# Kernel optimization log

Hardware: AMD Instinct MI355X
Metric: run time of the kernel (lower is better)

Reference implementation:

```python
import jax, jax.numpy as jnp
import numpy as np

N = 100000
E = 1600000
BN_EPS = 1e-5
# (in_channels, heads, out_channels, concat) per GATv2 layer
LAYERS = [(22, 3, 18, True), (54, 3, 14, True), (42, 3, 12, True), (36, 5, 10, False)]


def setup_inputs() -> dict:
    key = jax.random.key(0)
    ks = iter(jax.random.split(key, 64))
    nrm = lambda shape, s=0.1: jax.random.normal(next(ks), shape, jnp.float32) * s
    d = {}
    d["x"] = jax.random.normal(next(ks), (N, 22), jnp.float32)
    d["edge_index"] = jax.random.randint(next(ks), (2, E), 0, N)
    for i, (cin, h, c, concat) in enumerate(LAYERS, 1):
        d[f"Wl{i}"] = nrm((cin, h * c))
        d[f"Wr{i}"] = nrm((cin, h * c))
        d[f"bl{i}"] = jnp.zeros((h * c,), jnp.float32)
        d[f"br{i}"] = jnp.zeros((h * c,), jnp.float32)
        d[f"att{i}"] = nrm((h, c))
        outd = h * c if concat else c
        d[f"b{i}"] = jnp.zeros((outd,), jnp.float32)
        d[f"g{i}"] = jnp.ones((outd,), jnp.float32)
        d[f"be{i}"] = jnp.zeros((outd,), jnp.float32)
        d[f"rm{i}"] = nrm((outd,))
        d[f"rv{i}"] = jax.random.uniform(next(ks), (outd,), jnp.float32, 0.5, 1.5)
    d["Wmu"] = nrm((10, 10)); d["bmu"] = jnp.zeros((10,), jnp.float32)
    d["Wlv"] = nrm((10, 10)); d["blv"] = jnp.zeros((10,), jnp.float32)
    return d


def _gatv2(x, Wl, Wr, bl, br, att, b, src, dst, H, C, concat):
    n = x.shape[0]
    xl = (x @ Wl + bl).reshape(n, H, C)  # source transform (also the message)
    xr = (x @ Wr + br).reshape(n, H, C)  # target transform
    m = jax.nn.leaky_relu(xl[src] + xr[dst], 0.2)          # [Etot, H, C]
    e = jnp.einsum('ehc,hc->eh', m, att)                   # [Etot, H]
    emax = jax.lax.stop_gradient(jax.ops.segment_max(e, dst, num_segments=n))
    ex = jnp.exp(e - emax[dst])
    den = jax.ops.segment_sum(ex, dst, num_segments=n)     # [n, H]
    alpha = ex / den[dst]
    out = jax.ops.segment_sum(xl[src] * alpha[..., None], dst, num_segments=n)
    out = out.reshape(n, H * C) if concat else out.mean(axis=1)
    return out + b


def _bn(x, g, be, rm, rv):
    return g * (x - rm) * jax.lax.rsqrt(rv + BN_EPS) + be


def _fwd(p, edge_index):
    n = p["x"].shape[0]
    loop = jnp.arange(n)  # PyG GATv2Conv adds self-loops by default
    src = jnp.concatenate([edge_index[0], loop])
    dst = jnp.concatenate([edge_index[1], loop])
    h = p["x"]
    for i, (cin, H, C, concat) in enumerate(LAYERS, 1):
        h = _gatv2(h, p[f"Wl{i}"], p[f"Wr{i}"], p[f"bl{i}"], p[f"br{i}"],
                   p[f"att{i}"], p[f"b{i}"], src, dst, H, C, concat)
        h = _bn(h, p[f"g{i}"], p[f"be{i}"], p[f"rm{i}"], p[f"rv{i}"])
        if i == 1:  # source applies ELU only after bn1
            h = jax.nn.elu(h)
    mu = h @ p["Wmu"] + p["bmu"]
    log_var = h @ p["Wlv"] + p["blv"]
    return mu, log_var


def reference(x, edge_index, Wl1, Wr1, bl1, br1, att1, b1, g1, be1, rm1, rv1, Wl2, Wr2, bl2, br2, att2, b2, g2, be2, rm2, rv2, Wl3, Wr3, bl3, br3, att3, b3, g3, be3, rm3, rv3, Wl4, Wr4, bl4, br4, att4, b4, g4, be4, rm4, rv4, Wmu, bmu, Wlv, blv):
    p = {k: v for k, v in locals().items() if k != "edge_index"}
    return _fwd(p, edge_index)
```

## Files before the change

kernel.cpp:

```cpp
#include <hip/hip_runtime.h>

#define BN_EPS 1e-5f

typedef _Float16 half_t;
typedef _Float16 half2_t __attribute__((ext_vector_type(2)));

#define NBK_MAX 512
#define EPB 4096
#define REC 64
#define CAP 5120


__global__ void __launch_bounds__(256) bucket_scatter_kernel(
    const int* __restrict__ ei, int* __restrict__ bcur, int2* __restrict__ bstage,
    int E, int etot, int nbk) {
  __shared__ int2 se[EPB];
  __shared__ int lh[NBK_MAX], lbase[NBK_MAX];
  int base = blockIdx.x * EPB;
  int cnt = min(EPB, etot - base);
  for (int i = threadIdx.x; i < nbk; i += 256) lh[i] = 0;
  __syncthreads();
  for (int i = threadIdx.x; i < cnt; i += 256) {
    int e = base + i;
    int s, d;
    if (e < E) { s = ei[e]; d = ei[E + e]; } else { s = e - E; d = s; }
    se[i] = make_int2(s, d);
    atomicAdd(&lh[d >> 8], 1);
  }
  __syncthreads();
  for (int i = threadIdx.x; i < nbk; i += 256) {
    int c = lh[i];
    lbase[i] = c ? (i * CAP + atomicAdd(&bcur[i], c)) : 0;
    lh[i] = 0;
  }
  __syncthreads();
  for (int i = threadIdx.x; i < cnt; i += 256) {
    int2 sd = se[i];
    int b = sd.y >> 8;
    int r = atomicAdd(&lh[b], 1);
    bstage[lbase[b] + r] = sd;
  }
}

__global__ void __launch_bounds__(256) csr_finalize_kernel(
    const int2* __restrict__ bstage, const int* __restrict__ bcur,
    int* __restrict__ start, int* __restrict__ deg, int* __restrict__ csrc, int n) {
  __shared__ int ld[256];
  __shared__ int wsum[4];
  int b = blockIdx.x, tid = threadIdx.x;
  int d0 = b << 8;
  int p0 = b * CAP;
  int bc = bcur[b];
  ld[tid] = 0;
  __syncthreads();
  for (int p = p0 + tid; p < p0 + bc; p += 256)
    atomicAdd(&ld[bstage[p].y - d0], 1);
  __syncthreads();
  int v = ld[tid];
  int lane = tid & 63, wid = tid >> 6;
  int incl = v;
#pragma unroll
  for (int off = 1; off < 64; off <<= 1) {
    int t = __shfl_up(incl, off, 64);
    if (lane >= off) incl += t;
  }
  if (lane == 63) wsum[wid] = incl;
  __syncthreads();
  if (tid == 0) {
    int s = 0;
#pragma unroll
    for (int w = 0; w < 4; w++) { int t = wsum[w]; wsum[w] = s; s += t; }
  }
  __syncthreads();
  incl += wsum[wid];
  int st = p0 + incl - v;
  int i = d0 + tid;
  if (i < n) { start[i] = st; deg[i] = v; }
  __syncthreads();
  ld[tid] = st;
  __syncthreads();
  for (int p = p0 + tid; p < p0 + bc; p += 256) {
    int2 sd = bstage[p];
    int pos = atomicAdd(&ld[sd.y - d0], 1);
    csrc[pos] = sd.x;
  }
}


template <int CIN, int H, int C, int JT, typename IT>
__global__ void __launch_bounds__(256) transform_kernel(
    const IT* __restrict__ x, const float* __restrict__ Wl, const float* __restrict__ Wr,
    const float* __restrict__ bl, const float* __restrict__ br, half_t* __restrict__ xl,
    half_t* __restrict__ xr, int n) {
  constexpr int HC = H * C;
  constexpr int TPN = HC / JT;
  __shared__ float sW[2 * CIN * HC];
  for (int i = threadIdx.x; i < CIN * HC; i += blockDim.x) {
    sW[i] = Wl[i];
    sW[CIN * HC + i] = Wr[i];
  }
  __syncthreads();
  int idx = blockIdx.x * blockDim.x + threadIdx.x;
  if (idx >= n * TPN) return;
  int node = idx / TPN;
  int j0 = (idx - node * TPN) * JT;

  float al[JT], ar[JT];
#pragma unroll
  for (int jj = 0; jj < JT; jj++) {
    al[jj] = bl[j0 + jj];
    ar[jj] = br[j0 + jj];
  }
  float xrow[CIN];
  if constexpr (sizeof(IT) == 4) {
    const float2* xp = reinterpret_cast<const float2*>((const float*)x + (size_t)node * CIN);
#pragma unroll
    for (int k2 = 0; k2 < CIN / 2; k2++) {
      float2 v = xp[k2];
      xrow[2 * k2] = v.x;
      xrow[2 * k2 + 1] = v.y;
    }
  } else {
    const half2_t* xp = reinterpret_cast<const half2_t*>((const half_t*)x + (size_t)node * CIN);
#pragma unroll
    for (int k2 = 0; k2 < CIN / 2; k2++) {
      half2_t v = xp[k2];
      xrow[2 * k2] = (float)v.x;
      xrow[2 * k2 + 1] = (float)v.y;
    }
  }
#pragma unroll
  for (int k = 0; k < CIN; k++) {
    float xs = xrow[k];
#pragma unroll
    for (int jj = 0; jj < JT; jj++) {
      al[jj] = fmaf(xs, sW[k * HC + j0 + jj], al[jj]);
      ar[jj] = fmaf(xs, sW[CIN * HC + k * HC + j0 + jj], ar[jj]);
    }
  }
#pragma unroll
  for (int jj = 0; jj < JT; jj++) {
    int j = j0 + jj;
    xl[(size_t)node * REC + j] = (half_t)al[jj];
    xr[(size_t)node * HC + j] = (half_t)ar[jj];
  }
}


#define IDX(K) csrc[p0 + (((K) < cnt) ? (K) : cnt - 1)]

#define ROW(B, IR)                                                                  \
  {                                                                                 \
    const uint* xp_ = reinterpret_cast<const uint*>(xlh + (size_t)(IR) * REC);      \
    _Pragma("unroll") for (int i_ = 0; i_ < C2; i_++) B[i_] = xp_[i_];              \
  }

#define COMP_ROW(B, M)                                                                      \
  {                                                                                         \
    const half2_t* hp_ = reinterpret_cast<const half2_t*>(B);                               \
    float xs_[C];                                                                           \
    _Pragma("unroll") for (int i = 0; i < C2; i++) {                                        \
      xs_[2 * i] = (float)hp_[i].x;                                                         \
      xs_[2 * i + 1] = (float)hp_[i].y;                                                     \
    }                                                                                       \
    float e_ = 0.f;                                                                         \
    _Pragma("unroll") for (int c = 0; c < C; c++) {                                         \
      float m_ = xs_[c] + xr_reg[c];                                                        \
      m_ = (m_ > 0.f) ? m_ : 0.2f * m_;                                                     \
      e_ = fmaf(att_reg[c], m_, e_);                                                        \
    }                                                                                       \
    float ex_ = ((M) < cnt) ? __expf(e_) : 0.f;                                             \
    den += ex_;                                                                             \
    _Pragma("unroll") for (int c = 0; c < C; c++) acc[c] = fmaf(ex_, xs_[c], acc[c]);       \
  }

template <int H, int C, int MODE>
__global__ void __launch_bounds__(256) edge_kernel(
    const half_t* __restrict__ xl, const half_t* __restrict__ xr,
    const int* __restrict__ start, const int* __restrict__ deg,
    const int* __restrict__ csrc, const float* __restrict__ att,
    const float* __restrict__ bias, const float* __restrict__ g,
    const float* __restrict__ be, const float* __restrict__ rm,
    const float* __restrict__ rv, half_t* __restrict__ out, int n) {
  constexpr int HC = H * C;
  constexpr int C2 = C / 2;
  int t = blockIdx.x * blockDim.x + threadIdx.x;
  if (t >= n * H) return;
  int node = t / H;
  int h = t - node * H;

  float xr_reg[C], att_reg[C];
  const half2_t* xrp = reinterpret_cast<const half2_t*>(xr + (size_t)node * HC + h * C);
#pragma unroll
  for (int i = 0; i < C2; i++) {
    half2_t v = xrp[i];
    xr_reg[2 * i] = (float)v.x;
    xr_reg[2 * i + 1] = (float)v.y;
  }
#pragma unroll
  for (int c = 0; c < C; c++) att_reg[c] = att[h * C + c];

  float acc[C];
#pragma unroll
  for (int c = 0; c < C; c++) acc[c] = 0.f;
  float den = 0.f;

  int p0 = start[node];
  int cnt = deg[node];
  const half_t* xlh = xl + h * C;

  uint B0[C2], B1[C2], B2[C2];
  int i0, i1, i2;
  i0 = IDX(0); i1 = IDX(1); i2 = IDX(2);
  ROW(B0, i0) ROW(B1, i1) ROW(B2, i2)
  i0 = IDX(3); i1 = IDX(4); i2 = IDX(5);
  int cnt3 = ((cnt + 2) / 3) * 3;
  for (int m = 0; m < cnt3; m += 3) {
    COMP_ROW(B0, m)     ROW(B0, i0) i0 = IDX(m + 6);
    COMP_ROW(B1, m + 1) ROW(B1, i1) i1 = IDX(m + 7);
    COMP_ROW(B2, m + 2) ROW(B2, i2) i2 = IDX(m + 8);
  }

  float inv = 1.f / den;
  uint* orow = reinterpret_cast<uint*>(out + (size_t)node * HC + h * C);
#pragma unroll
  for (int c2 = 0; c2 < C2; c2++) {
    half2_t ov;
#pragma unroll
    for (int q = 0; q < 2; q++) {
      int c = 2 * c2 + q;
      float val = acc[c] * inv;
      if constexpr (MODE != 2) {
        int j = h * C + c;
        val += bias[j];
        float sc = g[j] * rsqrtf(rv[j] + BN_EPS);
        val = fmaf(sc, val - rm[j], be[j]);
        if constexpr (MODE == 1) val = (val > 0.f) ? val : expm1f(val);
      }
      if (q) ov.y = (half_t)val; else ov.x = (half_t)val;
    }
    orow[c2] = *reinterpret_cast<uint*>(&ov);
  }
}


__global__ void final_kernel(const half_t* __restrict__ r4, const float* __restrict__ b4,
                             const float* __restrict__ g4, const float* __restrict__ be4,
                             const float* __restrict__ rm4, const float* __restrict__ rv4,
                             const float* __restrict__ Wmu, const float* __restrict__ bmu,
                             const float* __restrict__ Wlv, const float* __restrict__ blv,
                             float* __restrict__ out, int n) {
  int node = blockIdx.x * blockDim.x + threadIdx.x;
  if (node >= n) return;
  float hsum[10];
#pragma unroll
  for (int c = 0; c < 10; c++) hsum[c] = 0.f;
  const half2_t* r = reinterpret_cast<const half2_t*>(r4 + (size_t)node * 50);
  float rv_[50];
#pragma unroll
  for (int i = 0; i < 25; i++) {
    half2_t v = r[i];
    rv_[2 * i] = (float)v.x;
    rv_[2 * i + 1] = (float)v.y;
  }
#pragma unroll
  for (int h = 0; h < 5; h++)
#pragma unroll
    for (int c = 0; c < 10; c++) hsum[c] += rv_[h * 10 + c];
  float hv[10];
#pragma unroll
  for (int c = 0; c < 10; c++) {
    float v = hsum[c] * 0.2f + b4[c];
    float sc = g4[c] * rsqrtf(rv4[c] + BN_EPS);
    hv[c] = fmaf(sc, v - rm4[c], be4[c]);
  }
#pragma unroll
  for (int j = 0; j < 10; j++) {
    float mu = bmu[j], lv = blv[j];
#pragma unroll
    for (int c = 0; c < 10; c++) {
      mu = fmaf(hv[c], Wmu[c * 10 + j], mu);
      lv = fmaf(hv[c], Wlv[c * 10 + j], lv);
    }
    out[(size_t)node * 10 + j] = mu;
    out[(size_t)n * 10 + (size_t)node * 10 + j] = lv;
  }
}


extern "C" void kernel_launch(void* const* d_in, const int* in_sizes, int n_in,
                              void* d_out, int out_size, void* d_ws, size_t ws_size,
                              hipStream_t stream) {
  const float* x = (const float*)d_in[0];
  const int* ei = (const int*)d_in[1];
  const int n = in_sizes[0] / 22;
  const int E = in_sizes[1] / 2;
  const int etot = E + n;
  const int nbk = (n + 255) >> 8;

  auto P = [&](int i) { return (const float*)d_in[i]; };

  char* ws = (char*)d_ws;
  size_t off = 0;
  auto alloc = [&](size_t bytes) -> void* {
    void* p = ws + off;
    off += (bytes + 255) & ~(size_t)255;
    return p;
  };
  half_t* xl = (half_t*)alloc((size_t)n * REC * 2);
  half_t* xr = (half_t*)alloc((size_t)n * 54 * 2);
  half_t* hb = (half_t*)alloc((size_t)n * 54 * 2);
  int* start = (int*)alloc((size_t)n * 4);
  int* deg = (int*)alloc((size_t)n * 4);
  int* csrc = (int*)alloc((size_t)nbk * CAP * 4);
  int* bcur = (int*)alloc((size_t)nbk * 4);
  int2* bstage = (int2*)xl;

  unsigned bb = (unsigned)((etot + EPB - 1) / EPB);
  unsigned nblk = (unsigned)((n + 255) / 256);

  hipMemsetAsync(bcur, 0, (size_t)nbk * 4, stream);
  bucket_scatter_kernel<<<bb, 256, 0, stream>>>(ei, bcur, bstage, E, etot, nbk);
  csr_finalize_kernel<<<(unsigned)nbk, 256, 0, stream>>>(bstage, bcur, start, deg, csrc, n);

  transform_kernel<22, 3, 18, 6, float><<<(unsigned)(((size_t)n * 9 + 255) / 256), 256, 0, stream>>>(
      x, P(2), P(3), P(4), P(5), xl, xr, n);
  edge_kernel<3, 18, 1><<<(unsigned)(((size_t)n * 3 + 255) / 256), 256, 0, stream>>>(
      xl, xr, start, deg, csrc, P(6), P(7), P(8), P(9), P(10), P(11), hb, n);

  transform_kernel<54, 3, 14, 6, half_t><<<(unsigned)(((size_t)n * 7 + 255) / 256), 256, 0, stream>>>(
      hb, P(12), P(13), P(14), P(15), xl, xr, n);
  edge_kernel<3, 14, 0><<<(unsigned)(((size_t)n * 3 + 255) / 256), 256, 0, stream>>>(
      xl, xr, start, deg, csrc, P(16), P(17), P(18), P(19), P(20), P(21), hb, n);

  transform_kernel<42, 3, 12, 6, half_t><<<(unsigned)(((size_t)n * 6 + 255) / 256), 256, 0, stream>>>(
      hb, P(22), P(23), P(24), P(25), xl, xr, n);
  edge_kernel<3, 12, 0><<<(unsigned)(((size_t)n * 3 + 255) / 256), 256, 0, stream>>>(
      xl, xr, start, deg, csrc, P(26), P(27), P(28), P(29), P(30), P(31), hb, n);

  transform_kernel<36, 5, 10, 10, half_t><<<(unsigned)(((size_t)n * 5 + 255) / 256), 256, 0, stream>>>(
      hb, P(32), P(33), P(34), P(35), xl, xr, n);
  edge_kernel<5, 10, 2><<<(unsigned)(((size_t)n * 5 + 255) / 256), 256, 0, stream>>>(
      xl, xr, start, deg, csrc, P(36), nullptr, nullptr, nullptr, nullptr, nullptr, hb, n);

  final_kernel<<<nblk, 256, 0, stream>>>(
      hb, P(37), P(38), P(39), P(40), P(41), P(42), P(43), P(44), P(45), (float*)d_out, n);
}
```

Before: 496.6 us.

## Use packed fp16 math in edge kernel and compact bucket staging

The edge kernel now does the leaky-relu, attention dot product (via fdot2) and the weighted accumulation in packed half2 arithmetic instead of converting each row to fp32. This cuts conversion and ALU work per edge. Accumulating in fp16 risks precision loss and overflow on high-degree nodes, because the exp weights are not normalised by a running max. The bucket scatter also drops its shared-memory staging in favour of reading edges twice from global memory, packs each (src, dst low byte) pair into one 32-bit word, and doubles the edges per block.

```diff
diff --git a/kernel.cpp b/kernel.cpp
--- a/kernel.cpp
+++ b/kernel.cpp
@@ -6,15 +6,20 @@
 typedef _Float16 half2_t __attribute__((ext_vector_type(2)));
 
 #define NBK_MAX 512
-#define EPB 4096
+#define EPB 8192
 #define REC 64
 #define CAP 5120
 
+#if __has_builtin(__builtin_amdgcn_fdot2)
+#define DOT2(a, b, c) __builtin_amdgcn_fdot2((a), (b), (c), false)
+#else
+#define DOT2(a, b, c) fmaf((float)(a).x, (float)(b).x, fmaf((float)(a).y, (float)(b).y, (c)))
+#endif
+
 
 __global__ void __launch_bounds__(256) bucket_scatter_kernel(
-    const int* __restrict__ ei, int* __restrict__ bcur, int2* __restrict__ bstage,
+    const int* __restrict__ ei, int* __restrict__ bcur, unsigned* __restrict__ bstage,
     int E, int etot, int nbk) {
-  __shared__ int2 se[EPB];
   __shared__ int lh[NBK_MAX], lbase[NBK_MAX];
   int base = blockIdx.x * EPB;
   int cnt = min(EPB, etot - base);
@@ -22,9 +27,7 @@
   __syncthreads();
   for (int i = threadIdx.x; i < cnt; i += 256) {
     int e = base + i;
-    int s, d;
-    if (e < E) { s = ei[e]; d = ei[E + e]; } else { s = e - E; d = s; }
-    se[i] = make_int2(s, d);
+    int d = (e < E) ? ei[E + e] : (e - E);
     atomicAdd(&lh[d >> 8], 1);
   }
   __syncthreads();
@@ -35,15 +38,17 @@
   }
   __syncthreads();
   for (int i = threadIdx.x; i < cnt; i += 256) {
-    int2 sd = se[i];
-    int b = sd.y >> 8;
+    int e = base + i;
+    int s, d;
+    if (e < E) { s = ei[e]; d = ei[E + e]; } else { s = e - E; d = s; }
+    int b = d >> 8;
     int r = atomicAdd(&lh[b], 1);
-    bstage[lbase[b] + r] = sd;
+    bstage[lbase[b] + r] = ((unsigned)s << 8) | (unsigned)(d & 255);
   }
 }
 
 __global__ void __launch_bounds__(256) csr_finalize_kernel(
-    const int2* __restrict__ bstage, const int* __restrict__ bcur,
+    const unsigned* __restrict__ bstage, const int* __restrict__ bcur,
     int* __restrict__ start, int* __restrict__ deg, int* __restrict__ csrc, int n) {
   __shared__ int ld[256];
   __shared__ int wsum[4];
@@ -54,7 +59,7 @@
   ld[tid] = 0;
   __syncthreads();
   for (int p = p0 + tid; p < p0 + bc; p += 256)
-    atomicAdd(&ld[bstage[p].y - d0], 1);
+    atomicAdd(&ld[bstage[p] & 255u], 1);
   __syncthreads();
   int v = ld[tid];
   int lane = tid & 63, wid = tid >> 6;
@@ -80,9 +85,9 @@
   ld[tid] = st;
   __syncthreads();
   for (int p = p0 + tid; p < p0 + bc; p += 256) {
-    int2 sd = bstage[p];
-    int pos = atomicAdd(&ld[sd.y - d0], 1);
-    csrc[pos] = sd.x;
+    unsigned sd = bstage[p];
+    int pos = atomicAdd(&ld[sd & 255u], 1);
+    csrc[pos] = (int)(sd >> 8);
   }
 }
 
@@ -155,23 +160,22 @@
     _Pragma("unroll") for (int i_ = 0; i_ < C2; i_++) B[i_] = xp_[i_];              \
   }
 
-#define COMP_ROW(B, M)                                                                      \
-  {                                                                                         \
-    const half2_t* hp_ = reinterpret_cast<const half2_t*>(B);                               \
-    float xs_[C];                                                                           \
-    _Pragma("unroll") for (int i = 0; i < C2; i++) {                                        \
-      xs_[2 * i] = (float)hp_[i].x;                                                         \
-      xs_[2 * i + 1] = (float)hp_[i].y;                                                     \
-    }                                                                                       \
-    float e_ = 0.f;                                                                         \
-    _Pragma("unroll") for (int c = 0; c < C; c++) {                                         \
-      float m_ = xs_[c] + xr_reg[c];                                                        \
-      m_ = (m_ > 0.f) ? m_ : 0.2f * m_;                                                     \
-      e_ = fmaf(att_reg[c], m_, e_);                                                        \
-    }                                                                                       \
-    float ex_ = ((M) < cnt) ? __expf(e_) : 0.f;                                             \
-    den += ex_;                                                                             \
-    _Pragma("unroll") for (int c = 0; c < C; c++) acc[c] = fmaf(ex_, xs_[c], acc[c]);       \
+#define COMP_ROW(B, M)                                                              \
+  {                                                                                 \
+    const half2_t* hp_ = reinterpret_cast<const half2_t*>(B);                       \
+    float e_ = 0.f;                                                                 \
+    _Pragma("unroll") for (int i = 0; i < C2; i++) {                                \
+      half2_t m_ = hp_[i] + xr_h[i];                                                \
+      half2_t mp_ = __builtin_elementwise_max(m_, h2z);                             \
+      half2_t mn_ = __builtin_elementwise_min(m_, h2z);                             \
+      m_ = mp_ + mn_ * h2lk;                                                        \
+      e_ = DOT2(att_h[i], m_, e_);                                                  \
+    }                                                                               \
+    float ex_ = ((M) < cnt) ? __expf(e_) : 0.f;                                     \
+    den += ex_;                                                                     \
+    half_t exs_ = (half_t)ex_;                                                      \
+    half2_t exv_ = {exs_, exs_};                                                    \
+    _Pragma("unroll") for (int i = 0; i < C2; i++) acc[i] += exv_ * hp_[i];         \
   }
 
 template <int H, int C, int MODE>
@@ -189,20 +193,17 @@
   int node = t / H;
   int h = t - node * H;
 
-  float xr_reg[C], att_reg[C];
+  const half2_t h2z = {(half_t)0.f, (half_t)0.f};
+  const half2_t h2lk = {(half_t)0.2f, (half_t)0.2f};
+
+  half2_t xr_h[C2], att_h[C2], acc[C2];
   const half2_t* xrp = reinterpret_cast<const half2_t*>(xr + (size_t)node * HC + h * C);
 #pragma unroll
   for (int i = 0; i < C2; i++) {
-    half2_t v = xrp[i];
-    xr_reg[2 * i] = (float)v.x;
-    xr_reg[2 * i + 1] = (float)v.y;
-  }
-#pragma unroll
-  for (int c = 0; c < C; c++) att_reg[c] = att[h * C + c];
-
-  float acc[C];
-#pragma unroll
-  for (int c = 0; c < C; c++) acc[c] = 0.f;
+    xr_h[i] = xrp[i];
+    att_h[i] = half2_t{(half_t)att[h * C + 2 * i], (half_t)att[h * C + 2 * i + 1]};
+    acc[i] = h2z;
+  }
   float den = 0.f;
 
   int p0 = start[node];
@@ -228,10 +229,10 @@
     half2_t ov;
 #pragma unroll
     for (int q = 0; q < 2; q++) {
-      int c = 2 * c2 + q;
-      float val = acc[c] * inv;
+      float a = q ? (float)acc[c2].y : (float)acc[c2].x;
+      float val = a * inv;
       if constexpr (MODE != 2) {
-        int j = h * C + c;
+        int j = h * C + 2 * c2 + q;
         val += bias[j];
         float sc = g[j] * rsqrtf(rv[j] + BN_EPS);
         val = fmaf(sc, val - rm[j], be[j]);
@@ -314,7 +315,7 @@
   int* deg = (int*)alloc((size_t)n * 4);
   int* csrc = (int*)alloc((size_t)nbk * CAP * 4);
   int* bcur = (int*)alloc((size_t)nbk * 4);
-  int2* bstage = (int2*)xl;
+  unsigned* bstage = (unsigned*)xl;
 
   unsigned bb = (unsigned)((etot + EPB - 1) / EPB);
   unsigned nblk = (unsigned)((n + 255) / 256);
```

New measurement: 478.8 us. -3.6%, faster.
